# Kernel tuning notes

Hardware: AMD Instinct MI355X
Metric: run time of the kernel (lower is better)

The kernel has to match this reference:

```python
import jax, jax.numpy as jnp
import numpy as np

N_NODES = 50000
N_EDGES = 800000
IN_C = 256
HID_C = 256
OUT_C = 128
N_GRAPHS = 256


def setup_inputs() -> dict:
    key = jax.random.key(0)
    ks = jax.random.split(key, 12)
    x = jax.random.normal(ks[0], (N_NODES, IN_C), dtype=jnp.float32)
    src = jax.random.randint(ks[1], (N_EDGES,), 0, N_NODES, dtype=jnp.int32)
    dst = jnp.sort(jax.random.randint(ks[2], (N_EDGES,), 0, N_NODES, dtype=jnp.int32))
    p = jax.random.uniform(ks[3], (N_NODES,), dtype=jnp.float32)
    batch = jnp.sort(jax.random.randint(ks[4], (N_NODES,), 0, N_GRAPHS, dtype=jnp.int32))
    root_ptr = jax.random.randint(ks[5], (N_GRAPHS,), 0, N_NODES, dtype=jnp.int32)
    s1 = 1.0 / np.sqrt(IN_C)
    s2 = 1.0 / np.sqrt(HID_C)
    s3 = 1.0 / np.sqrt(2 * HID_C)
    Wl1 = jax.random.uniform(ks[6], (IN_C, HID_C), jnp.float32, -s1, s1)
    Wr1 = jax.random.uniform(ks[7], (IN_C, HID_C), jnp.float32, -s1, s1)
    b1 = jnp.zeros((HID_C,), jnp.float32)
    Wl2 = jax.random.uniform(ks[8], (HID_C, HID_C), jnp.float32, -s2, s2)
    Wr2 = jax.random.uniform(ks[9], (HID_C, HID_C), jnp.float32, -s2, s2)
    b2 = jnp.zeros((HID_C,), jnp.float32)
    Wlin = jax.random.uniform(ks[10], (2 * HID_C, OUT_C), jnp.float32, -s3, s3)
    blin = jax.random.uniform(ks[11], (OUT_C,), jnp.float32, -s3, s3)
    return {"x": x, "src": src, "dst": dst, "p": p, "batch": batch,
            "root_ptr": root_ptr, "num_graphs": N_GRAPHS,
            "Wl1": Wl1, "Wr1": Wr1, "b1": b1,
            "Wl2": Wl2, "Wr2": Wr2, "b2": b2,
            "Wlin": Wlin, "blin": blin}


def _sage_conv(x, src, dst, inv_deg, Wl, Wr, b):
    # mean aggregation of neighbor features: scatter-add then divide by degree
    agg = jax.ops.segment_sum(x[src], dst, num_segments=N_NODES)  # [N, d]
    agg = agg * inv_deg[:, None]
    return agg @ Wl + x @ Wr + b


def reference(x, src, dst, p, batch, root_ptr, num_graphs,
              Wl1, Wr1, b1, Wl2, Wr2, b2, Wlin, blin):
    # in-degree for mean aggregation (shared by both convs)
    deg = jax.ops.segment_sum(jnp.ones_like(dst, dtype=x.dtype), dst,
                              num_segments=N_NODES)
    inv_deg = jnp.where(deg > 0, 1.0 / jnp.maximum(deg, 1.0), 0.0)

    h = _sage_conv(x, src, dst, inv_deg, Wl1, Wr1, b1)
    h = jax.nn.relu(h)  # dropout is identity in eval mode
    h = _sage_conv(h, src, dst, inv_deg, Wl2, Wr2, b2)

    # masked mean pool of p-weighted features per graph
    pw = h * p[:, None]
    gsum = jax.ops.segment_sum(pw, batch, num_segments=num_graphs)
    gcnt = jax.ops.segment_sum(jnp.ones_like(p), batch, num_segments=num_graphs)
    gmean = gsum / jnp.maximum(gcnt, 1.0)[:, None]

    feat = jnp.concatenate([h[root_ptr], gmean], axis=-1)  # [G, 2*hid]
    return feat @ Wlin + blin
```

## Files before the change

kernel.cpp:

```cpp
#include <hip/hip_runtime.h>
#include <hip/hip_bf16.h>

#define N_NODES 50000
#define N_EDGES 800000
#define C_DIM   256
#define OUT_C   128
#define N_GRAPHS 256

typedef unsigned short ushort8 __attribute__((ext_vector_type(8)));
typedef __bf16         bf16x8  __attribute__((ext_vector_type(8)));
typedef float          f32x4   __attribute__((ext_vector_type(4)));

__device__ __forceinline__ float us2f(unsigned short u) {
    unsigned int x = ((unsigned int)u) << 16;
    return __builtin_bit_cast(float, x);
}
__device__ __forceinline__ unsigned short f2bf(float f) {
    unsigned int u = __builtin_bit_cast(unsigned int, f);
    u += 0x7fffu + ((u >> 16) & 1u);
    return (unsigned short)(u >> 16);
}

__device__ __forceinline__ int lower_bound_i(const int* __restrict__ a, int n, int v) {
    int lo = 0, hi = n;
    while (lo < hi) {
        int mid = (lo + hi) >> 1;
        if (a[mid] < v) lo = mid + 1; else hi = mid;
    }
    return lo;
}

__global__ void build_ptrs(const int* __restrict__ dst, const int* __restrict__ batch,
                           int* __restrict__ row_ptr, int* __restrict__ graph_ptr,
                           float* __restrict__ inv_deg) {
    int i = blockIdx.x * blockDim.x + threadIdx.x;
    if (i <= N_NODES) {
        int lb = lower_bound_i(dst, N_EDGES, i);
        row_ptr[i] = lb;
        if (i < N_NODES) {
            int ub = lower_bound_i(dst, N_EDGES, i + 1);
            int cnt = ub - lb;
            inv_deg[i] = (cnt > 0) ? (1.0f / (float)cnt) : 0.0f;
        }
    }
    if (i <= N_GRAPHS) graph_ptr[i] = lower_bound_i(batch, N_NODES, i);
}

__global__ void convert_bf16(const float* __restrict__ S, unsigned short* __restrict__ D) {
    int i = blockIdx.x * blockDim.x + threadIdx.x;
    float4 v = *(const float4*)(S + ((size_t)i << 2));
    ushort4 o;
    o.x = f2bf(v.x); o.y = f2bf(v.y); o.z = f2bf(v.z); o.w = f2bf(v.w);
    *(ushort4*)(D + ((size_t)i << 2)) = o;
}

__global__ void transpose256x4(const float* __restrict__ S0, const float* __restrict__ S1,
                               const float* __restrict__ S2, const float* __restrict__ S3,
                               unsigned short* __restrict__ D0, unsigned short* __restrict__ D1,
                               unsigned short* __restrict__ D2, unsigned short* __restrict__ D3) {
    const float* S; unsigned short* D;
    switch (blockIdx.y) {
        case 0: S = S0; D = D0; break;
        case 1: S = S1; D = D1; break;
        case 2: S = S2; D = D2; break;
        default: S = S3; D = D3; break;
    }
    int i = blockIdx.x * 256 + threadIdx.x;
    int k = i >> 8, n = i & 255;
    D[n * 256 + k] = f2bf(S[i]);
}

__global__ void aggregate(const unsigned short* __restrict__ X,
                          const int* __restrict__ src,
                          const int* __restrict__ row_ptr,
                          const float* __restrict__ inv_deg,
                          unsigned short* __restrict__ out) {
    int gw   = (blockIdx.x * blockDim.x + threadIdx.x) >> 6;
    int lane = threadIdx.x & 63;
    if (gw >= N_NODES) return;
    int e0 = row_ptr[gw], e1 = row_ptr[gw + 1];
    float a0 = 0.f, a1 = 0.f, a2 = 0.f, a3 = 0.f;
    const int lo = lane << 2;
    int e = e0;
    for (; e + 8 <= e1; e += 8) {
        int s0 = src[e + 0], s1 = src[e + 1], s2 = src[e + 2], s3 = src[e + 3];
        int s4 = src[e + 4], s5 = src[e + 5], s6 = src[e + 6], s7 = src[e + 7];
        ushort4 v0 = *(const ushort4*)(X + ((size_t)s0 << 8) + lo);
        ushort4 v1 = *(const ushort4*)(X + ((size_t)s1 << 8) + lo);
        ushort4 v2 = *(const ushort4*)(X + ((size_t)s2 << 8) + lo);
        ushort4 v3 = *(const ushort4*)(X + ((size_t)s3 << 8) + lo);
        ushort4 v4 = *(const ushort4*)(X + ((size_t)s4 << 8) + lo);
        ushort4 v5 = *(const ushort4*)(X + ((size_t)s5 << 8) + lo);
        ushort4 v6 = *(const ushort4*)(X + ((size_t)s6 << 8) + lo);
        ushort4 v7 = *(const ushort4*)(X + ((size_t)s7 << 8) + lo);
        a0 += us2f(v0.x) + us2f(v1.x) + us2f(v2.x) + us2f(v3.x)
            + us2f(v4.x) + us2f(v5.x) + us2f(v6.x) + us2f(v7.x);
        a1 += us2f(v0.y) + us2f(v1.y) + us2f(v2.y) + us2f(v3.y)
            + us2f(v4.y) + us2f(v5.y) + us2f(v6.y) + us2f(v7.y);
        a2 += us2f(v0.z) + us2f(v1.z) + us2f(v2.z) + us2f(v3.z)
            + us2f(v4.z) + us2f(v5.z) + us2f(v6.z) + us2f(v7.z);
        a3 += us2f(v0.w) + us2f(v1.w) + us2f(v2.w) + us2f(v3.w)
            + us2f(v4.w) + us2f(v5.w) + us2f(v6.w) + us2f(v7.w);
    }
    for (; e < e1; ++e) {
        int s = src[e];
        ushort4 v = *(const ushort4*)(X + ((size_t)s << 8) + lo);
        a0 += us2f(v.x); a1 += us2f(v.y); a2 += us2f(v.z); a3 += us2f(v.w);
    }
    float sc = inv_deg[gw];
    ushort4 o;
    o.x = f2bf(a0 * sc); o.y = f2bf(a1 * sc); o.z = f2bf(a2 * sc); o.w = f2bf(a3 * sc);
    *(ushort4*)(out + ((size_t)gw << 8) + lo) = o;
}

__global__ __launch_bounds__(256, 2)
void gemm_fused(const unsigned short* __restrict__ A1,
                const unsigned short* __restrict__ A2,
                const unsigned short* __restrict__ B1t,
                const unsigned short* __restrict__ B2t,
                const float* __restrict__ bias,
                unsigned short* __restrict__ C,
                int M, int do_relu) {
    __shared__ __align__(16) unsigned short As[128][40];
    __shared__ __align__(16) unsigned short Bs[128][40];

    const int t    = threadIdx.x;
    const int m0   = blockIdx.x * 128;
    const int n0   = blockIdx.y * 128;
    const int lane = t & 63, wid = t >> 6;
    const int wm   = (wid >> 1) * 64;
    const int wn   = (wid & 1) * 64;
    const int lrow = lane & 15;
    const int koff = (lane >> 4) * 8;

    const f32x4 zero4 = {0.f, 0.f, 0.f, 0.f};
    f32x4 acc[4][4];
#pragma unroll
    for (int i = 0; i < 4; ++i)
#pragma unroll
        for (int j = 0; j < 4; ++j) acc[i][j] = zero4;

    const ushort8 zero8 = {0, 0, 0, 0, 0, 0, 0, 0};

    for (int it = 0; it < 16; ++it) {
        int kt = it * 32;
        const unsigned short* __restrict__ Ab = (kt < 256) ? A1 : A2;
        const unsigned short* __restrict__ Bb = (kt < 256) ? B1t : B2t;
        int ko = kt & 255;

#pragma unroll
        for (int i = 0; i < 2; ++i) {
            int idx = (t + i * 256) * 8;
            int r = idx >> 5, c = idx & 31;
            int gr = m0 + r;
            ushort8 va = zero8;
            if (gr < M) va = *(const ushort8*)(Ab + (size_t)gr * 256 + ko + c);
            *(ushort8*)&As[r][c] = va;
            int gn = n0 + r;
            ushort8 vb = *(const ushort8*)(Bb + (size_t)gn * 256 + ko + c);
            *(ushort8*)&Bs[r][c] = vb;
        }
        __syncthreads();

        bf16x8 af[4], bfr[4];
#pragma unroll
        for (int mi = 0; mi < 4; ++mi) {
            uint4 u = *(const uint4*)&As[wm + mi * 16 + lrow][koff];
            af[mi] = __builtin_bit_cast(bf16x8, u);
        }
#pragma unroll
        for (int ni = 0; ni < 4; ++ni) {
            uint4 u = *(const uint4*)&Bs[wn + ni * 16 + lrow][koff];
            bfr[ni] = __builtin_bit_cast(bf16x8, u);
        }
#pragma unroll
        for (int mi = 0; mi < 4; ++mi)
#pragma unroll
            for (int ni = 0; ni < 4; ++ni)
                acc[mi][ni] = __builtin_amdgcn_mfma_f32_16x16x32_bf16(
                    af[mi], bfr[ni], acc[mi][ni], 0, 0, 0);
        __syncthreads();
    }

    const int rbase = (lane >> 4) * 4;
#pragma unroll
    for (int ni = 0; ni < 4; ++ni) {
        int n  = n0 + wn + ni * 16 + lrow;
        float bv = bias[n];
#pragma unroll
        for (int mi = 0; mi < 4; ++mi) {
            int mb = m0 + wm + mi * 16 + rbase;
#pragma unroll
            for (int r = 0; r < 4; ++r) {
                int m = mb + r;
                if (m < M) {
                    float v = acc[mi][ni][r] + bv;
                    if (do_relu) v = fmaxf(v, 0.f);
                    C[(size_t)m * 256 + n] = f2bf(v);
                }
            }
        }
    }
}

__global__ void pool_feat(const unsigned short* __restrict__ h2,
                          const float* __restrict__ p,
                          const int* __restrict__ graph_ptr,
                          const int* __restrict__ root_ptr,
                          float* __restrict__ feat) {
    int g = blockIdx.x;
    int c = threadIdx.x;
    int s = graph_ptr[g], e = graph_ptr[g + 1];
    float acc = 0.f;
    for (int n = s; n < e; ++n) {
        float pv = p[n];
        acc += us2f(h2[(size_t)n * 256 + c]) * pv;
    }
    float cnt = (float)(e - s);
    float gmean = acc / fmaxf(cnt, 1.0f);
    int root = root_ptr[g];
    feat[(size_t)g * 512 + c]       = us2f(h2[(size_t)root * 256 + c]);
    feat[(size_t)g * 512 + 256 + c] = gmean;
}

__global__ void final_gemm(const float* __restrict__ feat,
                           const float* __restrict__ Wlin,
                           const float* __restrict__ blin,
                           float* __restrict__ out) {
    int g = blockIdx.x;
    int o = threadIdx.x;
    __shared__ float fl[512];
    for (int k = o; k < 512; k += 128) fl[k] = feat[(size_t)g * 512 + k];
    __syncthreads();
    float acc = blin[o];
    for (int k = 0; k < 512; ++k)
        acc += fl[k] * Wlin[k * 128 + o];
    out[(size_t)g * 128 + o] = acc;
}

extern "C" void kernel_launch(void* const* d_in, const int* in_sizes, int n_in,
                              void* d_out, int out_size, void* d_ws, size_t ws_size,
                              hipStream_t stream) {
    const float* x        = (const float*)d_in[0];
    const int*   src      = (const int*)d_in[1];
    const int*   dst      = (const int*)d_in[2];
    const float* p        = (const float*)d_in[3];
    const int*   batch    = (const int*)d_in[4];
    const int*   root_ptr = (const int*)d_in[5];
    const float* Wl1  = (const float*)d_in[7];
    const float* Wr1  = (const float*)d_in[8];
    const float* b1   = (const float*)d_in[9];
    const float* Wl2  = (const float*)d_in[10];
    const float* Wr2  = (const float*)d_in[11];
    const float* b2   = (const float*)d_in[12];
    const float* Wlin = (const float*)d_in[13];
    const float* blin = (const float*)d_in[14];
    float* out = (float*)d_out;

    size_t off = 0;
    char* base = (char*)d_ws;
    auto alloc = [&](size_t bytes) -> void* {
        void* q = base + off;
        off += (bytes + 255) & ~(size_t)255;
        return q;
    };
    int*            row_ptr   = (int*)  alloc((N_NODES + 1) * sizeof(int));
    int*            graph_ptr = (int*)  alloc((N_GRAPHS + 1) * sizeof(int));
    float*          inv_deg   = (float*)alloc(N_NODES * sizeof(float));
    unsigned short* Wl1t = (unsigned short*)alloc(256 * 256 * 2);
    unsigned short* Wr1t = (unsigned short*)alloc(256 * 256 * 2);
    unsigned short* Wl2t = (unsigned short*)alloc(256 * 256 * 2);
    unsigned short* Wr2t = (unsigned short*)alloc(256 * 256 * 2);
    unsigned short* xb   = (unsigned short*)alloc((size_t)N_NODES * 256 * 2);
    unsigned short* aggb = (unsigned short*)alloc((size_t)N_NODES * 256 * 2);
    unsigned short* h1   = (unsigned short*)alloc((size_t)N_NODES * 256 * 2);
    unsigned short* h2   = (unsigned short*)alloc((size_t)N_NODES * 256 * 2);
    float*          feat = (float*)alloc((size_t)N_GRAPHS * 512 * sizeof(float));
    (void)ws_size; (void)n_in; (void)in_sizes; (void)out_size;

    build_ptrs<<<196, 256, 0, stream>>>(dst, batch, row_ptr, graph_ptr, inv_deg);
    convert_bf16<<<N_NODES * 256 / 4 / 256, 256, 0, stream>>>(x, xb);
    transpose256x4<<<dim3(256, 4), 256, 0, stream>>>(Wl1, Wr1, Wl2, Wr2,
                                                     Wl1t, Wr1t, Wl2t, Wr2t);

    dim3 ggrid((N_NODES + 127) / 128, 2);

    aggregate<<<N_NODES / 4, 256, 0, stream>>>(xb, src, row_ptr, inv_deg, aggb);
    gemm_fused<<<ggrid, 256, 0, stream>>>(aggb, xb, Wl1t, Wr1t, b1, h1, N_NODES, 1);

    aggregate<<<N_NODES / 4, 256, 0, stream>>>(h1, src, row_ptr, inv_deg, aggb);
    gemm_fused<<<ggrid, 256, 0, stream>>>(aggb, h1, Wl2t, Wr2t, b2, h2, N_NODES, 0);

    pool_feat<<<N_GRAPHS, 256, 0, stream>>>(h2, p, graph_ptr, root_ptr, feat);
    final_gemm<<<N_GRAPHS, 128, 0, stream>>>(feat, Wlin, blin, out);
}
```

Before: 392.9 us.

## Deepen gather batching, use direct global-to-LDS loads in GEMM, unroll pool and head

The neighbor aggregation now issues 16 independent row gathers per iteration and handles the remainder with clamped, zero-weighted gathers instead of a serial tail loop. The fused GEMM stages tiles with global_load_lds straight into a k-major shared-memory layout, dropping the register round trip and the row-bounds check. The pooling kernel batches 8 node loads with masked weights, and the final linear layer uses four independent accumulators. Together these aim to raise memory-level parallelism and cut staging overhead. The risks are higher register pressure, possible LDS bank conflicts from the new layout, and out-of-bounds reads in the last GEMM row block now that the M guard is gone.

```diff
diff --git a/kernel.cpp b/kernel.cpp
--- a/kernel.cpp
+++ b/kernel.cpp
@@ -10,6 +10,9 @@
 typedef unsigned short ushort8 __attribute__((ext_vector_type(8)));
 typedef __bf16         bf16x8  __attribute__((ext_vector_type(8)));
 typedef float          f32x4   __attribute__((ext_vector_type(4)));
+
+typedef __attribute__((address_space(1))) const unsigned int gu32;
+typedef __attribute__((address_space(3))) unsigned int lu32;
 
 __device__ __forceinline__ float us2f(unsigned short u) {
     unsigned int x = ((unsigned int)u) << 16;
@@ -79,34 +82,62 @@
     int lane = threadIdx.x & 63;
     if (gw >= N_NODES) return;
     int e0 = row_ptr[gw], e1 = row_ptr[gw + 1];
+    const int lo = lane << 2;
     float a0 = 0.f, a1 = 0.f, a2 = 0.f, a3 = 0.f;
-    const int lo = lane << 2;
     int e = e0;
-    for (; e + 8 <= e1; e += 8) {
-        int s0 = src[e + 0], s1 = src[e + 1], s2 = src[e + 2], s3 = src[e + 3];
-        int s4 = src[e + 4], s5 = src[e + 5], s6 = src[e + 6], s7 = src[e + 7];
-        ushort4 v0 = *(const ushort4*)(X + ((size_t)s0 << 8) + lo);
-        ushort4 v1 = *(const ushort4*)(X + ((size_t)s1 << 8) + lo);
-        ushort4 v2 = *(const ushort4*)(X + ((size_t)s2 << 8) + lo);
-        ushort4 v3 = *(const ushort4*)(X + ((size_t)s3 << 8) + lo);
-        ushort4 v4 = *(const ushort4*)(X + ((size_t)s4 << 8) + lo);
-        ushort4 v5 = *(const ushort4*)(X + ((size_t)s5 << 8) + lo);
-        ushort4 v6 = *(const ushort4*)(X + ((size_t)s6 << 8) + lo);
-        ushort4 v7 = *(const ushort4*)(X + ((size_t)s7 << 8) + lo);
-        a0 += us2f(v0.x) + us2f(v1.x) + us2f(v2.x) + us2f(v3.x)
-            + us2f(v4.x) + us2f(v5.x) + us2f(v6.x) + us2f(v7.x);
-        a1 += us2f(v0.y) + us2f(v1.y) + us2f(v2.y) + us2f(v3.y)
-            + us2f(v4.y) + us2f(v5.y) + us2f(v6.y) + us2f(v7.y);
-        a2 += us2f(v0.z) + us2f(v1.z) + us2f(v2.z) + us2f(v3.z)
-            + us2f(v4.z) + us2f(v5.z) + us2f(v6.z) + us2f(v7.z);
-        a3 += us2f(v0.w) + us2f(v1.w) + us2f(v2.w) + us2f(v3.w)
-            + us2f(v4.w) + us2f(v5.w) + us2f(v6.w) + us2f(v7.w);
-    }
-    for (; e < e1; ++e) {
-        int s = src[e];
-        ushort4 v = *(const ushort4*)(X + ((size_t)s << 8) + lo);
-        a0 += us2f(v.x); a1 += us2f(v.y); a2 += us2f(v.z); a3 += us2f(v.w);
-    }
+
+    for (; e + 16 <= e1; e += 16) {
+        ushort4 v[16];
+#pragma unroll
+        for (int j = 0; j < 16; ++j) {
+            int s = src[e + j];
+            v[j] = *(const ushort4*)(X + ((size_t)s << 8) + lo);
+        }
+#pragma unroll
+        for (int j = 0; j < 16; ++j) {
+            a0 += us2f(v[j].x); a1 += us2f(v[j].y);
+            a2 += us2f(v[j].z); a3 += us2f(v[j].w);
+        }
+    }
+    int rem = e1 - e;
+    if (rem > 8) {
+        int cl = e1 - 1;
+        ushort4 v[16]; float w[16];
+#pragma unroll
+        for (int j = 0; j < 16; ++j) {
+            int ej = e + j;
+            int ec = ej < cl ? ej : cl;
+            w[j] = (ej < e1) ? 1.0f : 0.0f;
+            int s = src[ec];
+            v[j] = *(const ushort4*)(X + ((size_t)s << 8) + lo);
+        }
+#pragma unroll
+        for (int j = 0; j < 16; ++j) {
+            a0 = fmaf(us2f(v[j].x), w[j], a0);
+            a1 = fmaf(us2f(v[j].y), w[j], a1);
+            a2 = fmaf(us2f(v[j].z), w[j], a2);
+            a3 = fmaf(us2f(v[j].w), w[j], a3);
+        }
+    } else if (rem > 0) {
+        int cl = e1 - 1;
+        ushort4 v[8]; float w[8];
+#pragma unroll
+        for (int j = 0; j < 8; ++j) {
+            int ej = e + j;
+            int ec = ej < cl ? ej : cl;
+            w[j] = (ej < e1) ? 1.0f : 0.0f;
+            int s = src[ec];
+            v[j] = *(const ushort4*)(X + ((size_t)s << 8) + lo);
+        }
+#pragma unroll
+        for (int j = 0; j < 8; ++j) {
+            a0 = fmaf(us2f(v[j].x), w[j], a0);
+            a1 = fmaf(us2f(v[j].y), w[j], a1);
+            a2 = fmaf(us2f(v[j].z), w[j], a2);
+            a3 = fmaf(us2f(v[j].w), w[j], a3);
+        }
+    }
+
     float sc = inv_deg[gw];
     ushort4 o;
     o.x = f2bf(a0 * sc); o.y = f2bf(a1 * sc); o.z = f2bf(a2 * sc); o.w = f2bf(a3 * sc);
@@ -121,8 +152,8 @@
                 const float* __restrict__ bias,
                 unsigned short* __restrict__ C,
                 int M, int do_relu) {
-    __shared__ __align__(16) unsigned short As[128][40];
-    __shared__ __align__(16) unsigned short Bs[128][40];
+    __shared__ __align__(16) unsigned short As[4096];
+    __shared__ __align__(16) unsigned short Bs[4096];
 
     const int t    = threadIdx.x;
     const int m0   = blockIdx.x * 128;
@@ -131,7 +162,7 @@
     const int wm   = (wid >> 1) * 64;
     const int wn   = (wid & 1) * 64;
     const int lrow = lane & 15;
-    const int koff = (lane >> 4) * 8;
+    const int kq   = lane >> 4;
 
     const f32x4 zero4 = {0.f, 0.f, 0.f, 0.f};
     f32x4 acc[4][4];
@@ -139,8 +170,6 @@
     for (int i = 0; i < 4; ++i)
 #pragma unroll
         for (int j = 0; j < 4; ++j) acc[i][j] = zero4;
-
-    const ushort8 zero8 = {0, 0, 0, 0, 0, 0, 0, 0};
 
     for (int it = 0; it < 16; ++it) {
         int kt = it * 32;
@@ -150,27 +179,25 @@
 
 #pragma unroll
         for (int i = 0; i < 2; ++i) {
-            int idx = (t + i * 256) * 8;
-            int r = idx >> 5, c = idx & 31;
-            int gr = m0 + r;
-            ushort8 va = zero8;
-            if (gr < M) va = *(const ushort8*)(Ab + (size_t)gr * 256 + ko + c);
-            *(ushort8*)&As[r][c] = va;
-            int gn = n0 + r;
-            ushort8 vb = *(const ushort8*)(Bb + (size_t)gn * 256 + ko + c);
-            *(ushort8*)&Bs[r][c] = vb;
+            int q   = t + i * 256;
+            int row = q & 127;
+            int kb  = q >> 7;
+            const unsigned short* ga = Ab + (size_t)(m0 + row) * 256 + ko + kb * 8;
+            __builtin_amdgcn_global_load_lds((gu32*)ga, (lu32*)(As + q * 8), 16, 0, 0);
+            const unsigned short* gb = Bb + (size_t)(n0 + row) * 256 + ko + kb * 8;
+            __builtin_amdgcn_global_load_lds((gu32*)gb, (lu32*)(Bs + q * 8), 16, 0, 0);
         }
         __syncthreads();
 
         bf16x8 af[4], bfr[4];
 #pragma unroll
         for (int mi = 0; mi < 4; ++mi) {
-            uint4 u = *(const uint4*)&As[wm + mi * 16 + lrow][koff];
+            uint4 u = *(const uint4*)(As + ((kq * 128) + wm + mi * 16 + lrow) * 8);
             af[mi] = __builtin_bit_cast(bf16x8, u);
         }
 #pragma unroll
         for (int ni = 0; ni < 4; ++ni) {
-            uint4 u = *(const uint4*)&Bs[wn + ni * 16 + lrow][koff];
+            uint4 u = *(const uint4*)(Bs + ((kq * 128) + wn + ni * 16 + lrow) * 8);
             bfr[ni] = __builtin_bit_cast(bf16x8, u);
         }
 #pragma unroll
@@ -212,9 +239,19 @@
     int c = threadIdx.x;
     int s = graph_ptr[g], e = graph_ptr[g + 1];
     float acc = 0.f;
-    for (int n = s; n < e; ++n) {
-        float pv = p[n];
-        acc += us2f(h2[(size_t)n * 256 + c]) * pv;
+    for (int n = s; n < e; n += 8) {
+        int cl = e - 1;
+        unsigned short v[8]; float w[8];
+#pragma unroll
+        for (int j = 0; j < 8; ++j) {
+            int nj = n + j;
+            int nc = nj < cl ? nj : cl;
+            w[j] = (nj < e) ? p[nc] : 0.0f;
+            v[j] = h2[(size_t)nc * 256 + c];
+        }
+#pragma unroll
+        for (int j = 0; j < 8; ++j)
+            acc = fmaf(us2f(v[j]), w[j], acc);
     }
     float cnt = (float)(e - s);
     float gmean = acc / fmaxf(cnt, 1.0f);
@@ -232,10 +269,14 @@
     __shared__ float fl[512];
     for (int k = o; k < 512; k += 128) fl[k] = feat[(size_t)g * 512 + k];
     __syncthreads();
-    float acc = blin[o];
-    for (int k = 0; k < 512; ++k)
-        acc += fl[k] * Wlin[k * 128 + o];
-    out[(size_t)g * 128 + o] = acc;
+    float s0 = 0.f, s1 = 0.f, s2 = 0.f, s3 = 0.f;
+    for (int k = 0; k < 512; k += 4) {
+        s0 = fmaf(fl[k + 0], Wlin[(k + 0) * 128 + o], s0);
+        s1 = fmaf(fl[k + 1], Wlin[(k + 1) * 128 + o], s1);
+        s2 = fmaf(fl[k + 2], Wlin[(k + 2) * 128 + o], s2);
+        s3 = fmaf(fl[k + 3], Wlin[(k + 3) * 128 + o], s3);
+    }
+    out[(size_t)g * 128 + o] = blin[o] + ((s0 + s1) + (s2 + s3));
 }
 
 extern "C" void kernel_launch(void* const* d_in, const int* in_sizes, int n_in,
```

New measurement: 380.6 us. -3.1%, faster.
